# Performance work log

Hardware: AMD Instinct MI355X
Metric: run time of the kernel (lower is better)

## Reference

```python
import jax, jax.numpy as jnp
import numpy as np


def sym_logm(x):
    # matrix log of symmetric positive-definite matrices via eigh
    w, v = jnp.linalg.eigh(x)
    return jnp.einsum('...ik,...k,...jk->...ij', v, jnp.log(w), v)


def olm_diffeo(x):
    s = sym_logm(x)
    L = jnp.tril(s, -1)
    return L + L.swapaxes(-1, -2)


def cayley_map(X):
    I = jnp.eye(X.shape[-1], dtype=X.dtype)
    return (I - X) @ jnp.linalg.inv(I + X)


def trans_base(W, y):
    # C = cayley(skew(W)); y -> sym off-diagonal part of C y C^T
    C = cayley_map(W - W.T)
    y = jnp.einsum('pq,bnqr,sr->bnps', C, y, C)
    L = jnp.tril(y, -1)
    return L + L.swapaxes(-1, -2)


def setup_inputs() -> dict:
    B, N, n = 16, 512, 32
    key = jax.random.key(0)
    k1, k2, k3, k4 = jax.random.split(key, 4)
    A = jax.random.normal(k1, (B, N, n, n), dtype=jnp.float32)
    cov = A @ A.swapaxes(-1, -2) / n + jnp.eye(n, dtype=jnp.float32)
    d = jnp.sqrt(jnp.diagonal(cov, axis1=-2, axis2=-1))
    x = cov / (d[..., :, None] * d[..., None, :])  # SPD correlation matrices
    q_weight = jax.random.normal(k2, (n, n), dtype=jnp.float32) * 2.0 - 1.0
    k_weight = jax.random.normal(k3, (n, n), dtype=jnp.float32) * 2.0 - 1.0
    v_weight = jax.random.normal(k4, (n, n), dtype=jnp.float32) * 2.0 - 1.0
    return {"x": x, "q_weight": q_weight, "k_weight": k_weight, "v_weight": v_weight}


def reference(x, q_weight, k_weight, v_weight):
    xl = olm_diffeo(x)                       # [B,N,n,n]
    q = trans_base(q_weight, xl)
    k = trans_base(k_weight, xl)
    v = trans_base(v_weight, xl)
    B, N, n, _ = q.shape
    qf = q.reshape(B, N, n * n)
    kf = k.reshape(B, N, n * n)
    # energy[b,j,i] = ||q_i - k_j||_F  (Gram trick instead of [B,N,N,n,n] broadcast)
    q2 = jnp.sum(qf * qf, axis=-1)
    k2 = jnp.sum(kf * kf, axis=-1)
    d2 = q2[:, None, :] + k2[:, :, None] - 2.0 * jnp.einsum('bjf,bif->bji', kf, qf)
    energy = jnp.sqrt(jnp.maximum(d2, 1e-12))
    scores = 1.0 / (1.0 + jnp.log1p(energy))
    p = jax.nn.softmax(scores, axis=-2)      # softmax over j (dim -2), as in torch
    attn = p.swapaxes(-1, -2)                # [b, i, j]
    # out[b,c] = sum_a v[b,a] * attn[b,a,c]  (faithful to torch broadcast+sum(dim=1))
    return jnp.einsum('bac,baij->bcij', attn, v)
```

## Files before the change

kernel.cpp:

```cpp
#include <hip/hip_runtime.h>
#include <math.h>

#define NB 16
#define NSQ 512
#define NMAT (NB*NSQ)
#define NF 1024
#define NSWEEP 7
#define SB 36

__global__ __launch_bounds__(64) void cayley_kernel(
    const float* __restrict__ qw, const float* __restrict__ kw,
    const float* __restrict__ vw, float* __restrict__ Cout) {
  __shared__ float M[32][33];
  __shared__ float R[32][33];
  __shared__ float fac[32];
  const float* W = (blockIdx.x == 0) ? qw : ((blockIdx.x == 1) ? kw : vw);
  const int t = threadIdx.x;
  for (int idx = t; idx < 1024; idx += 64) {
    int i = idx >> 5, j = idx & 31;
    float xv = W[i*32+j] - W[j*32+i];
    float d = (i == j) ? 1.0f : 0.0f;
    M[i][j] = d - xv;
    R[i][j] = d + xv;
  }
  __syncthreads();
  for (int k = 0; k < 32; ++k) {
    float inv = 1.0f / M[k][k];
    __syncthreads();
    if (t < 32) M[k][t] *= inv; else R[k][t-32] *= inv;
    __syncthreads();
    if (t < 32) fac[t] = M[t][k];
    __syncthreads();
    if (t < 32) {
      float mk = M[k][t];
      for (int i = 0; i < 32; ++i) {
        if (i == k) continue;
        M[i][t] -= fac[i] * mk;
      }
    } else {
      int tc = t - 32;
      float rk = R[k][tc];
      for (int i = 0; i < 32; ++i) {
        if (i == k) continue;
        R[i][tc] -= fac[i] * rk;
      }
    }
    __syncthreads();
  }
  for (int idx = t; idx < 1024; idx += 64) {
    int p = idx >> 5, q = idx & 31;
    Cout[blockIdx.x * 1024 + idx] = R[q][p];
  }
}

__global__ __launch_bounds__(128) void logm_qkv_kernel(
    const float* __restrict__ x, const float* __restrict__ Cm,
    float* __restrict__ qo, float* __restrict__ ko, float* __restrict__ vo,
    float* __restrict__ q2, float* __restrict__ k2) {
  __shared__ __align__(16) float buf0[32*SB];
  __shared__ __align__(16) float buf1[32*SB];
  __shared__ __align__(16) float buf2[32*SB];
  __shared__ __align__(16) float2 cs[16];
  __shared__ __align__(16) float lw[32];
  __shared__ float wsum[2];
  const int t = threadIdx.x;
  const int m = blockIdx.x;
  const float* xm = x + (size_t)m * NF;

  #pragma unroll
  for (int s = 0; s < 2; ++s) {
    int fi = t + 128*s;
    int i = fi >> 3, j4 = (fi & 7) << 2;
    float4 xv = *(const float4*)&xm[(size_t)fi*4];
    *(float4*)&buf0[i*SB + j4] = xv;
    float4 iv;
    iv.x = (i == j4+0) ? 1.0f : 0.0f;
    iv.y = (i == j4+1) ? 1.0f : 0.0f;
    iv.z = (i == j4+2) ? 1.0f : 0.0f;
    iv.w = (i == j4+3) ? 1.0f : 0.0f;
    *(float4*)&buf1[i*SB + j4] = iv;
  }
  __syncthreads();

  const int abase = t >> 4;
  const int bI = t & 15;
  const int pi = abase & 1;

  for (int sw = 0; sw < NSWEEP; ++sw) {
    for (int r = 1; r < 32; ++r) {
      const int h = 31 - __builtin_clz((unsigned)r);
      const int lowmask = (1 << h) - 1;
      if (t < 16) {
        int p = ((t >> h) << (h+1)) | (t & lowmask);
        int q = p ^ r;
        float apq = buf0[p*SB+q];
        float c = 1.0f, s = 0.0f;
        if (fabsf(apq) > 1e-36f) {
          float app = buf0[p*SB+p];
          float aqq = buf0[q*SB+q];
          float tau = (aqq - app) / (2.0f * apq);
          float tt = 1.0f / (fabsf(tau) + sqrtf(1.0f + tau*tau));
          tt = (tau < 0.0f) ? -tt : tt;
          c = 1.0f / sqrtf(1.0f + tt*tt);
          s = tt * c;
        }
        cs[t] = make_float2(c, s);
      }
      __syncthreads();
      if (r == 1) {
        {
          int pr = t >> 3;
          int ch = (t & 7) << 2;
          int p = pr << 1;
          int q = p | 1;
          float2 c2 = cs[pr];
          float4 ap = *(float4*)&buf0[p*SB + ch];
          float4 aq = *(float4*)&buf0[q*SB + ch];
          float4 np, nq;
          np.x = c2.x*ap.x - c2.y*aq.x;  nq.x = fmaf(c2.y, ap.x, c2.x*aq.x);
          np.y = c2.x*ap.y - c2.y*aq.y;  nq.y = fmaf(c2.y, ap.y, c2.x*aq.y);
          np.z = c2.x*ap.z - c2.y*aq.z;  nq.z = fmaf(c2.y, ap.z, c2.x*aq.z);
          np.w = c2.x*ap.w - c2.y*aq.w;  nq.w = fmaf(c2.y, ap.w, c2.x*aq.w);
          *(float4*)&buf0[p*SB + ch] = np;
          *(float4*)&buf0[q*SB + ch] = nq;
        }
        __syncthreads();
        #pragma unroll
        for (int s4 = 0; s4 < 2; ++s4) {
          int tsk = t + 128*s4;
          int i = tsk >> 3;
          int cch = tsk & 7;
          float2 cA = cs[2*cch];
          float2 cB = cs[2*cch+1];
          float4 y = *(float4*)&buf0[i*SB + 4*cch];
          float4 z;
          z.x = cA.x*y.x - cA.y*y.y;  z.y = fmaf(cA.y, y.x, cA.x*y.y);
          z.z = cB.x*y.z - cB.y*y.w;  z.w = fmaf(cB.y, y.z, cB.x*y.w);
          *(float4*)&buf0[i*SB + 4*cch] = z;
        }
      } else {
        int pb = ((bI >> h) << (h+1)) | (bI & lowmask);
        int qb = pb ^ r;
        if (pi) { int tmp = pb; pb = qb; qb = tmp; }
        const float2 cb2 = cs[bI];
        const float cbb = cb2.x;
        const float sbb = pi ? -cb2.y : cb2.y;
        #pragma unroll
        for (int u = 0; u < 2; ++u) {
          int a = abase + 8*u;
          int pa = ((a >> h) << (h+1)) | (a & lowmask);
          int qa = pa ^ r;
          if (pi) { int tmp = pa; pa = qa; qa = tmp; }
          float2 ca2 = cs[a];
          float caa = ca2.x;
          float saa = pi ? -ca2.y : ca2.y;
          float* rp = buf0 + pa*SB;
          float* rq = buf0 + qa*SB;
          float x11 = rp[pb], x12 = rp[qb];
          float x21 = rq[pb], x22 = rq[qb];
          float y11 = caa*x11 - saa*x21;
          float y12 = caa*x12 - saa*x22;
          float y21 = fmaf(saa, x11, caa*x21);
          float y22 = fmaf(saa, x12, caa*x22);
          rp[pb] = cbb*y11 - sbb*y12;
          rp[qb] = fmaf(sbb, y11, cbb*y12);
          rq[pb] = cbb*y21 - sbb*y22;
          rq[qb] = fmaf(sbb, y21, cbb*y22);
        }
      }
      {
        int pr = t >> 3;
        int ch = (t & 7) << 2;
        int p = ((pr >> h) << (h+1)) | (pr & lowmask);
        int q = p ^ r;
        float2 c2 = cs[pr];
        float4 vp = *(float4*)&buf1[p*SB + ch];
        float4 vq = *(float4*)&buf1[q*SB + ch];
        float4 np, nq;
        np.x = c2.x*vp.x - c2.y*vq.x;  nq.x = fmaf(c2.y, vp.x, c2.x*vq.x);
        np.y = c2.x*vp.y - c2.y*vq.y;  nq.y = fmaf(c2.y, vp.y, c2.x*vq.y);
        np.z = c2.x*vp.z - c2.y*vq.z;  nq.z = fmaf(c2.y, vp.z, c2.x*vq.z);
        np.w = c2.x*vp.w - c2.y*vq.w;  nq.w = fmaf(c2.y, vp.w, c2.x*vq.w);
        *(float4*)&buf1[p*SB + ch] = np;
        *(float4*)&buf1[q*SB + ch] = nq;
      }
      __syncthreads();
    }
  }

  if (t < 32) lw[t] = logf(fmaxf(buf0[t*SB+t], 1e-30f));
  __syncthreads();
  #pragma unroll
  for (int s = 0; s < 8; ++s) {
    int idx = t + 128*s;
    int i = idx >> 5, k = idx & 31;
    buf0[i*SB + k] = buf1[k*SB + i];
  }
  __syncthreads();

  const int rg = t >> 4, cg = t & 15;
  const int i0 = rg*4, j0 = cg*2;
  {
    float acc[4][2] = {};
    #pragma unroll
    for (int k4 = 0; k4 < 32; k4 += 4) {
      float4 lv = *(float4*)&lw[k4];
      float4 av[4], bv[2];
      #pragma unroll
      for (int d = 0; d < 4; ++d) {
        float4 a4 = *(float4*)&buf0[(i0+d)*SB + k4];
        av[d].x = a4.x*lv.x; av[d].y = a4.y*lv.y; av[d].z = a4.z*lv.z; av[d].w = a4.w*lv.w;
      }
      #pragma unroll
      for (int e = 0; e < 2; ++e)
        bv[e] = *(float4*)&buf0[(j0+e)*SB + k4];
      #pragma unroll
      for (int d = 0; d < 4; ++d)
        #pragma unroll
        for (int e = 0; e < 2; ++e) {
          acc[d][e] = fmaf(av[d].x, bv[e].x, acc[d][e]);
          acc[d][e] = fmaf(av[d].y, bv[e].y, acc[d][e]);
          acc[d][e] = fmaf(av[d].z, bv[e].z, acc[d][e]);
          acc[d][e] = fmaf(av[d].w, bv[e].w, acc[d][e]);
        }
    }
    #pragma unroll
    for (int d = 0; d < 4; ++d) {
      #pragma unroll
      for (int e = 0; e < 2; ++e)
        if (i0+d == j0+e) acc[d][e] = 0.0f;
      float2 z; z.x = acc[d][0]; z.y = acc[d][1];
      *(float2*)&buf1[(i0+d)*SB + j0] = z;
    }
  }
  __syncthreads();

  for (int w = 0; w < 3; ++w) {
    const float* Cw = Cm + w*1024;
    #pragma unroll
    for (int s = 0; s < 2; ++s) {
      int fi = t + 128*s;
      int i = fi >> 3, c4 = (fi & 7) << 2;
      *(float4*)&buf0[i*SB + c4] = *(const float4*)&Cw[fi*4];
    }
    __syncthreads();
    {
      float acc[4][2] = {};
      #pragma unroll
      for (int k4 = 0; k4 < 32; k4 += 4) {
        float4 av[4], bv[2];
        #pragma unroll
        for (int d = 0; d < 4; ++d)
          av[d] = *(float4*)&buf0[(i0+d)*SB + k4];
        #pragma unroll
        for (int e = 0; e < 2; ++e)
          bv[e] = *(float4*)&buf1[(j0+e)*SB + k4];
        #pragma unroll
        for (int d = 0; d < 4; ++d)
          #pragma unroll
          for (int e = 0; e < 2; ++e) {
            acc[d][e] = fmaf(av[d].x, bv[e].x, acc[d][e]);
            acc[d][e] = fmaf(av[d].y, bv[e].y, acc[d][e]);
            acc[d][e] = fmaf(av[d].z, bv[e].z, acc[d][e]);
            acc[d][e] = fmaf(av[d].w, bv[e].w, acc[d][e]);
          }
      }
      #pragma unroll
      for (int d = 0; d < 4; ++d) {
        float2 z; z.x = acc[d][0]; z.y = acc[d][1];
        *(float2*)&buf2[(i0+d)*SB + j0] = z;
      }
    }
    __syncthreads();
    {
      float acc[4][2] = {};
      #pragma unroll
      for (int k4 = 0; k4 < 32; k4 += 4) {
        float4 av[4], bv[2];
        #pragma unroll
        for (int d = 0; d < 4; ++d)
          av[d] = *(float4*)&buf2[(i0+d)*SB + k4];
        #pragma unroll
        for (int e = 0; e < 2; ++e)
          bv[e] = *(float4*)&buf0[(j0+e)*SB + k4];
        #pragma unroll
        for (int d = 0; d < 4; ++d)
          #pragma unroll
          for (int e = 0; e < 2; ++e) {
            acc[d][e] = fmaf(av[d].x, bv[e].x, acc[d][e]);
            acc[d][e] = fmaf(av[d].y, bv[e].y, acc[d][e]);
            acc[d][e] = fmaf(av[d].z, bv[e].z, acc[d][e]);
            acc[d][e] = fmaf(av[d].w, bv[e].w, acc[d][e]);
          }
      }
      float ss = 0.0f;
      float* outp = (w == 0) ? qo : ((w == 1) ? ko : vo);
      #pragma unroll
      for (int d = 0; d < 4; ++d) {
        #pragma unroll
        for (int e = 0; e < 2; ++e) {
          if (i0+d == j0+e) acc[d][e] = 0.0f;
          ss = fmaf(acc[d][e], acc[d][e], ss);
        }
        float2 z; z.x = acc[d][0]; z.y = acc[d][1];
        *(float2*)&outp[(size_t)m*NF + (i0+d)*32 + j0] = z;
      }
      if (w < 2) {
        #pragma unroll
        for (int off = 32; off > 0; off >>= 1)
          ss += __shfl_down(ss, off);
        if ((t & 63) == 0) wsum[t >> 6] = ss;
      }
      __syncthreads();
      if (w < 2 && t == 0)
        ((w == 0) ? q2 : k2)[m] = wsum[0] + wsum[1];
    }
  }
}

__global__ __launch_bounds__(256) void scores_kernel(
    const float* __restrict__ qf, const float* __restrict__ kf,
    const float* __restrict__ q2, const float* __restrict__ k2,
    float* __restrict__ P) {
  __shared__ float Ks[16][132];
  __shared__ float Qs[16][132];
  const int b = blockIdx.z;
  const int j0 = blockIdx.y * 128;
  const int i0 = blockIdx.x * 128;
  const int tx = threadIdx.x & 15, ty = threadIdx.x >> 4;
  const int srow = threadIdx.x >> 1;
  const int sk8  = (threadIdx.x & 1) * 8;
  float acc[8][8] = {};
  const float* kb = kf + (size_t)(b*NSQ + j0) * NF;
  const float* qb = qf + (size_t)(b*NSQ + i0) * NF;
  for (int f0 = 0; f0 < NF; f0 += 16) {
    float4 ka = *(const float4*)(kb + (size_t)srow*NF + f0 + sk8);
    float4 kb4 = *(const float4*)(kb + (size_t)srow*NF + f0 + sk8 + 4);
    float4 qa = *(const float4*)(qb + (size_t)srow*NF + f0 + sk8);
    float4 qb4 = *(const float4*)(qb + (size_t)srow*NF + f0 + sk8 + 4);
    __syncthreads();
    Ks[sk8+0][srow] = ka.x;  Ks[sk8+1][srow] = ka.y;
    Ks[sk8+2][srow] = ka.z;  Ks[sk8+3][srow] = ka.w;
    Ks[sk8+4][srow] = kb4.x; Ks[sk8+5][srow] = kb4.y;
    Ks[sk8+6][srow] = kb4.z; Ks[sk8+7][srow] = kb4.w;
    Qs[sk8+0][srow] = qa.x;  Qs[sk8+1][srow] = qa.y;
    Qs[sk8+2][srow] = qa.z;  Qs[sk8+3][srow] = qa.w;
    Qs[sk8+4][srow] = qb4.x; Qs[sk8+5][srow] = qb4.y;
    Qs[sk8+6][srow] = qb4.z; Qs[sk8+7][srow] = qb4.w;
    __syncthreads();
    #pragma unroll
    for (int kk = 0; kk < 16; ++kk) {
      float4 a0 = *(float4*)&Ks[kk][ty*8];
      float4 a1 = *(float4*)&Ks[kk][ty*8 + 4];
      float4 b0 = *(float4*)&Qs[kk][tx*8];
      float4 b1 = *(float4*)&Qs[kk][tx*8 + 4];
      float av[8] = {a0.x,a0.y,a0.z,a0.w,a1.x,a1.y,a1.z,a1.w};
      float bv[8] = {b0.x,b0.y,b0.z,b0.w,b1.x,b1.y,b1.z,b1.w};
      #pragma unroll
      for (int d = 0; d < 8; ++d)
        #pragma unroll
        for (int e = 0; e < 8; ++e)
          acc[d][e] = fmaf(av[d], bv[e], acc[d][e]);
    }
  }
  #pragma unroll
  for (int u = 0; u < 8; ++u) {
    int j = j0 + ty*8 + u;
    float kj = k2[b*NSQ + j];
    float* prow = P + (size_t)(b*NSQ + j)*NSQ + i0 + tx*8;
    #pragma unroll
    for (int vv = 0; vv < 8; ++vv) {
      int i = i0 + tx*8 + vv;
      float d2 = kj + q2[b*NSQ + i] - 2.0f * acc[u][vv];
      float e = sqrtf(fmaxf(d2, 1e-12f));
      prow[vv] = 1.0f / (1.0f + log1pf(e));
    }
  }
}

__global__ __launch_bounds__(512) void softmax_kernel(float* __restrict__ P) {
  __shared__ float red[16][32];
  const int b = blockIdx.x >> 4;
  const int i0 = (blockIdx.x & 15) * 32;
  const int il = threadIdx.x & 31;
  const int jg = threadIdx.x >> 5;
  float* base = P + (size_t)b*NSQ*NSQ + i0 + il;
  float mx = -1e30f;
  for (int j = jg*32; j < jg*32 + 32; ++j)
    mx = fmaxf(mx, base[(size_t)j*NSQ]);
  red[jg][il] = mx;
  __syncthreads();
  float cm = red[0][il];
  #pragma unroll
  for (int g = 1; g < 16; ++g) cm = fmaxf(cm, red[g][il]);
  __syncthreads();
  float ssum = 0.0f;
  for (int j = jg*32; j < jg*32 + 32; ++j)
    ssum += expf(base[(size_t)j*NSQ] - cm);
  red[jg][il] = ssum;
  __syncthreads();
  float tot = red[0][il];
  #pragma unroll
  for (int g = 1; g < 16; ++g) tot += red[g][il];
  float inv = 1.0f / tot;
  for (int j = jg*32; j < jg*32 + 32; ++j) {
    size_t o = (size_t)j*NSQ;
    base[o] = expf(base[o] - cm) * inv;
  }
}

__global__ __launch_bounds__(256) void out_gemm_kernel(
    const float* __restrict__ P, const float* __restrict__ vf,
    float* __restrict__ out) {
  __shared__ float Ps[16][132];
  __shared__ float Vs[16][132];
  const int b = blockIdx.z;
  const int c0 = blockIdx.y * 128;
  const int f0 = blockIdx.x * 128;
  const int tx = threadIdx.x & 15, ty = threadIdx.x >> 4;
  const int srow = threadIdx.x >> 1;
  const int sk8  = (threadIdx.x & 1) * 8;
  const int vrow = threadIdx.x >> 4;
  const int vc8  = (threadIdx.x & 15) * 8;
  float acc[8][8] = {};
  const float* Pb = P + (size_t)b * NSQ * NSQ;
  const float* Vb = vf + (size_t)b * NSQ * NF;
  for (int a0 = 0; a0 < NSQ; a0 += 16) {
    float4 pa = *(const float4*)(Pb + (size_t)(c0 + srow)*NSQ + a0 + sk8);
    float4 pb4 = *(const float4*)(Pb + (size_t)(c0 + srow)*NSQ + a0 + sk8 + 4);
    float4 va = *(const float4*)(Vb + (size_t)(a0 + vrow)*NF + f0 + vc8);
    float4 vb4 = *(const float4*)(Vb + (size_t)(a0 + vrow)*NF + f0 + vc8 + 4);
    __syncthreads();
    Ps[sk8+0][srow] = pa.x;  Ps[sk8+1][srow] = pa.y;
    Ps[sk8+2][srow] = pa.z;  Ps[sk8+3][srow] = pa.w;
    Ps[sk8+4][srow] = pb4.x; Ps[sk8+5][srow] = pb4.y;
    Ps[sk8+6][srow] = pb4.z; Ps[sk8+7][srow] = pb4.w;
    *(float4*)&Vs[vrow][vc8] = va;
    *(float4*)&Vs[vrow][vc8 + 4] = vb4;
    __syncthreads();
    #pragma unroll
    for (int kk = 0; kk < 16; ++kk) {
      float4 a0v = *(float4*)&Ps[kk][ty*8];
      float4 a1v = *(float4*)&Ps[kk][ty*8 + 4];
      float4 b0v = *(float4*)&Vs[kk][tx*8];
      float4 b1v = *(float4*)&Vs[kk][tx*8 + 4];
      float av[8] = {a0v.x,a0v.y,a0v.z,a0v.w,a1v.x,a1v.y,a1v.z,a1v.w};
      float bv[8] = {b0v.x,b0v.y,b0v.z,b0v.w,b1v.x,b1v.y,b1v.z,b1v.w};
      #pragma unroll
      for (int d = 0; d < 8; ++d)
        #pragma unroll
        for (int e = 0; e < 8; ++e)
          acc[d][e] = fmaf(av[d], bv[e], acc[d][e]);
    }
  }
  #pragma unroll
  for (int u = 0; u < 8; ++u) {
    float* orow = out + (size_t)(b*NSQ + c0 + ty*8 + u) * NF + f0 + tx*8;
    float4 o0; o0.x = acc[u][0]; o0.y = acc[u][1]; o0.z = acc[u][2]; o0.w = acc[u][3];
    float4 o1; o1.x = acc[u][4]; o1.y = acc[u][5]; o1.z = acc[u][6]; o1.w = acc[u][7];
    *(float4*)orow = o0;
    *(float4*)(orow + 4) = o1;
  }
}

extern "C" void kernel_launch(void* const* d_in, const int* in_sizes, int n_in,
                              void* d_out, int out_size, void* d_ws, size_t ws_size,
                              hipStream_t stream) {
  const float* x  = (const float*)d_in[0];
  const float* qw = (const float*)d_in[1];
  const float* kw = (const float*)d_in[2];
  const float* vw = (const float*)d_in[3];
  float* ws = (float*)d_ws;
  float* C  = ws;
  float* q  = ws + 3072;
  float* k  = q + (size_t)NMAT * NF;
  float* v  = k + (size_t)NMAT * NF;
  float* q2 = v + (size_t)NMAT * NF;
  float* k2 = q2 + NMAT;
  float* P  = k2 + NMAT;
  float* out = (float*)d_out;

  cayley_kernel<<<dim3(3), dim3(64), 0, stream>>>(qw, kw, vw, C);
  logm_qkv_kernel<<<dim3(NMAT), dim3(128), 0, stream>>>(x, C, q, k, v, q2, k2);
  scores_kernel<<<dim3(4, 4, NB), dim3(256), 0, stream>>>(q, k, q2, k2, P);
  softmax_kernel<<<dim3(NB * 16), dim3(512), 0, stream>>>(P);
  out_gemm_kernel<<<dim3(8, 4, NB), dim3(256), 0, stream>>>(P, v, out);
}
```

Measured before the change: 1.532 ms.

## Shrink logm_qkv blocks to one wavefront and read Cayley matrices from global

The per-matrix Jacobi/logm/QKV kernel now runs with 64 threads (a single wavefront) per matrix instead of 128, so each thread does twice the rotation and GEMM work with 4x4 register tiles. The Cayley matrices are read straight from global memory (cached) rather than staged into shared memory, which drops one shared buffer and a barrier per projection. The norm reduction no longer needs a cross-wave shared-memory step. Fewer threads per block cuts shared memory per block and lets more blocks fit per CU, but it raises per-thread serial work inside the barrier-heavy sweep loop.

```diff
diff --git a/kernel.cpp b/kernel.cpp
--- a/kernel.cpp
+++ b/kernel.cpp
@@ -53,23 +53,21 @@
   }
 }
 
-__global__ __launch_bounds__(128) void logm_qkv_kernel(
+__global__ __launch_bounds__(64) void logm_qkv_kernel(
     const float* __restrict__ x, const float* __restrict__ Cm,
     float* __restrict__ qo, float* __restrict__ ko, float* __restrict__ vo,
     float* __restrict__ q2, float* __restrict__ k2) {
   __shared__ __align__(16) float buf0[32*SB];
   __shared__ __align__(16) float buf1[32*SB];
-  __shared__ __align__(16) float buf2[32*SB];
   __shared__ __align__(16) float2 cs[16];
   __shared__ __align__(16) float lw[32];
-  __shared__ float wsum[2];
   const int t = threadIdx.x;
   const int m = blockIdx.x;
   const float* xm = x + (size_t)m * NF;
 
   #pragma unroll
-  for (int s = 0; s < 2; ++s) {
-    int fi = t + 128*s;
+  for (int s = 0; s < 4; ++s) {
+    int fi = t + 64*s;
     int i = fi >> 3, j4 = (fi & 7) << 2;
     float4 xv = *(const float4*)&xm[(size_t)fi*4];
     *(float4*)&buf0[i*SB + j4] = xv;
@@ -108,9 +106,11 @@
       }
       __syncthreads();
       if (r == 1) {
-        {
-          int pr = t >> 3;
-          int ch = (t & 7) << 2;
+        #pragma unroll
+        for (int s2 = 0; s2 < 2; ++s2) {
+          int tk = t + 64*s2;
+          int pr = tk >> 3;
+          int ch = (tk & 7) << 2;
           int p = pr << 1;
           int q = p | 1;
           float2 c2 = cs[pr];
@@ -126,8 +126,8 @@
         }
         __syncthreads();
         #pragma unroll
-        for (int s4 = 0; s4 < 2; ++s4) {
-          int tsk = t + 128*s4;
+        for (int s4 = 0; s4 < 4; ++s4) {
+          int tsk = t + 64*s4;
           int i = tsk >> 3;
           int cch = tsk & 7;
           float2 cA = cs[2*cch];
@@ -146,8 +146,8 @@
         const float cbb = cb2.x;
         const float sbb = pi ? -cb2.y : cb2.y;
         #pragma unroll
-        for (int u = 0; u < 2; ++u) {
-          int a = abase + 8*u;
+        for (int u = 0; u < 4; ++u) {
+          int a = abase + 4*u;
           int pa = ((a >> h) << (h+1)) | (a & lowmask);
           int qa = pa ^ r;
           if (pi) { int tmp = pa; pa = qa; qa = tmp; }
@@ -168,9 +168,11 @@
           rq[qb] = fmaf(sbb, y21, cbb*y22);
         }
       }
-      {
-        int pr = t >> 3;
-        int ch = (t & 7) << 2;
+      #pragma unroll
+      for (int s2 = 0; s2 < 2; ++s2) {
+        int tk = t + 64*s2;
+        int pr = tk >> 3;
+        int ch = (tk & 7) << 2;
         int p = ((pr >> h) << (h+1)) | (pr & lowmask);
         int q = p ^ r;
         float2 c2 = cs[pr];
@@ -191,33 +193,33 @@
   if (t < 32) lw[t] = logf(fmaxf(buf0[t*SB+t], 1e-30f));
   __syncthreads();
   #pragma unroll
-  for (int s = 0; s < 8; ++s) {
-    int idx = t + 128*s;
+  for (int s = 0; s < 16; ++s) {
+    int idx = t + 64*s;
     int i = idx >> 5, k = idx & 31;
     buf0[i*SB + k] = buf1[k*SB + i];
   }
   __syncthreads();
 
-  const int rg = t >> 4, cg = t & 15;
-  const int i0 = rg*4, j0 = cg*2;
+  const int rg = t >> 3, cg = t & 7;
+  const int i0 = rg*4, j0 = cg*4;
   {
-    float acc[4][2] = {};
+    float acc[4][4] = {};
     #pragma unroll
     for (int k4 = 0; k4 < 32; k4 += 4) {
       float4 lv = *(float4*)&lw[k4];
-      float4 av[4], bv[2];
+      float4 av[4], bv[4];
       #pragma unroll
       for (int d = 0; d < 4; ++d) {
         float4 a4 = *(float4*)&buf0[(i0+d)*SB + k4];
         av[d].x = a4.x*lv.x; av[d].y = a4.y*lv.y; av[d].z = a4.z*lv.z; av[d].w = a4.w*lv.w;
       }
       #pragma unroll
-      for (int e = 0; e < 2; ++e)
+      for (int e = 0; e < 4; ++e)
         bv[e] = *(float4*)&buf0[(j0+e)*SB + k4];
       #pragma unroll
       for (int d = 0; d < 4; ++d)
         #pragma unroll
-        for (int e = 0; e < 2; ++e) {
+        for (int e = 0; e < 4; ++e) {
           acc[d][e] = fmaf(av[d].x, bv[e].x, acc[d][e]);
           acc[d][e] = fmaf(av[d].y, bv[e].y, acc[d][e]);
           acc[d][e] = fmaf(av[d].z, bv[e].z, acc[d][e]);
@@ -227,38 +229,32 @@
     #pragma unroll
     for (int d = 0; d < 4; ++d) {
       #pragma unroll
-      for (int e = 0; e < 2; ++e)
+      for (int e = 0; e < 4; ++e)
         if (i0+d == j0+e) acc[d][e] = 0.0f;
-      float2 z; z.x = acc[d][0]; z.y = acc[d][1];
-      *(float2*)&buf1[(i0+d)*SB + j0] = z;
+      float4 z4;
+      z4.x = acc[d][0]; z4.y = acc[d][1]; z4.z = acc[d][2]; z4.w = acc[d][3];
+      *(float4*)&buf1[(i0+d)*SB + j0] = z4;
     }
   }
   __syncthreads();
 
   for (int w = 0; w < 3; ++w) {
     const float* Cw = Cm + w*1024;
-    #pragma unroll
-    for (int s = 0; s < 2; ++s) {
-      int fi = t + 128*s;
-      int i = fi >> 3, c4 = (fi & 7) << 2;
-      *(float4*)&buf0[i*SB + c4] = *(const float4*)&Cw[fi*4];
-    }
-    __syncthreads();
     {
-      float acc[4][2] = {};
+      float acc[4][4] = {};
       #pragma unroll
       for (int k4 = 0; k4 < 32; k4 += 4) {
-        float4 av[4], bv[2];
+        float4 av[4], bv[4];
         #pragma unroll
         for (int d = 0; d < 4; ++d)
-          av[d] = *(float4*)&buf0[(i0+d)*SB + k4];
-        #pragma unroll
-        for (int e = 0; e < 2; ++e)
+          av[d] = *(const float4*)&Cw[(i0+d)*32 + k4];
+        #pragma unroll
+        for (int e = 0; e < 4; ++e)
           bv[e] = *(float4*)&buf1[(j0+e)*SB + k4];
         #pragma unroll
         for (int d = 0; d < 4; ++d)
           #pragma unroll
-          for (int e = 0; e < 2; ++e) {
+          for (int e = 0; e < 4; ++e) {
             acc[d][e] = fmaf(av[d].x, bv[e].x, acc[d][e]);
             acc[d][e] = fmaf(av[d].y, bv[e].y, acc[d][e]);
             acc[d][e] = fmaf(av[d].z, bv[e].z, acc[d][e]);
@@ -267,26 +263,27 @@
       }
       #pragma unroll
       for (int d = 0; d < 4; ++d) {
-        float2 z; z.x = acc[d][0]; z.y = acc[d][1];
-        *(float2*)&buf2[(i0+d)*SB + j0] = z;
+        float4 z4;
+        z4.x = acc[d][0]; z4.y = acc[d][1]; z4.z = acc[d][2]; z4.w = acc[d][3];
+        *(float4*)&buf0[(i0+d)*SB + j0] = z4;
       }
     }
     __syncthreads();
     {
-      float acc[4][2] = {};
+      float acc[4][4] = {};
       #pragma unroll
       for (int k4 = 0; k4 < 32; k4 += 4) {
-        float4 av[4], bv[2];
+        float4 av[4], bv[4];
         #pragma unroll
         for (int d = 0; d < 4; ++d)
-          av[d] = *(float4*)&buf2[(i0+d)*SB + k4];
-        #pragma unroll
-        for (int e = 0; e < 2; ++e)
-          bv[e] = *(float4*)&buf0[(j0+e)*SB + k4];
+          av[d] = *(float4*)&buf0[(i0+d)*SB + k4];
+        #pragma unroll
+        for (int e = 0; e < 4; ++e)
+          bv[e] = *(const float4*)&Cw[(j0+e)*32 + k4];
         #pragma unroll
         for (int d = 0; d < 4; ++d)
           #pragma unroll
-          for (int e = 0; e < 2; ++e) {
+          for (int e = 0; e < 4; ++e) {
             acc[d][e] = fmaf(av[d].x, bv[e].x, acc[d][e]);
             acc[d][e] = fmaf(av[d].y, bv[e].y, acc[d][e]);
             acc[d][e] = fmaf(av[d].z, bv[e].z, acc[d][e]);
@@ -298,22 +295,22 @@
       #pragma unroll
       for (int d = 0; d < 4; ++d) {
         #pragma unroll
-        for (int e = 0; e < 2; ++e) {
+        for (int e = 0; e < 4; ++e) {
           if (i0+d == j0+e) acc[d][e] = 0.0f;
           ss = fmaf(acc[d][e], acc[d][e], ss);
         }
-        float2 z; z.x = acc[d][0]; z.y = acc[d][1];
-        *(float2*)&outp[(size_t)m*NF + (i0+d)*32 + j0] = z;
+        float4 z4;
+        z4.x = acc[d][0]; z4.y = acc[d][1]; z4.z = acc[d][2]; z4.w = acc[d][3];
+        *(float4*)&outp[(size_t)m*NF + (i0+d)*32 + j0] = z4;
       }
       if (w < 2) {
         #pragma unroll
         for (int off = 32; off > 0; off >>= 1)
           ss += __shfl_down(ss, off);
-        if ((t & 63) == 0) wsum[t >> 6] = ss;
+        if (t == 0)
+          ((w == 0) ? q2 : k2)[m] = ss;
       }
       __syncthreads();
-      if (w < 2 && t == 0)
-        ((w == 0) ? q2 : k2)[m] = wsum[0] + wsum[1];
     }
   }
 }
@@ -481,7 +478,7 @@
   float* out = (float*)d_out;
 
   cayley_kernel<<<dim3(3), dim3(64), 0, stream>>>(qw, kw, vw, C);
-  logm_qkv_kernel<<<dim3(NMAT), dim3(128), 0, stream>>>(x, C, q, k, v, q2, k2);
+  logm_qkv_kernel<<<dim3(NMAT), dim3(64), 0, stream>>>(x, C, q, k, v, q2, k2);
   scores_kernel<<<dim3(4, 4, NB), dim3(256), 0, stream>>>(q, k, q2, k2, P);
   softmax_kernel<<<dim3(NB * 16), dim3(512), 0, stream>>>(P);
   out_gemm_kernel<<<dim3(8, 4, NB), dim3(256), 0, stream>>>(P, v, out);
```

New measurement: 1.461 ms. 4.6% less time.
